# Kernel tuning notes

Hardware: AMD Instinct MI355X
Metric: run time of the kernel (lower is better)

The kernel has to match this reference:

```python
import jax, jax.numpy as jnp
import numpy as np

# Forest of complete L-ary trees, BFS level-contiguous node numbering.
B_TREES, ARITY, DEPTH = 8, 4, 8
C, M, NGEN = 8, 100, 4
COUNTS = [B_TREES * ARITY**l for l in range(DEPTH + 1)]
OFFS = np.concatenate([[0], np.cumsum(COUNTS)]).astype(np.int64)
DIM = int(OFFS[-1])  # 699048
# tree id of each node: within-level index // (ARITY**level)
BATCH = np.concatenate([np.arange(COUNTS[l]) // (ARITY**l) for l in range(DEPTH + 1)])


def setup_inputs() -> dict:
    key = jax.random.key(0)
    k1, k2, k3, k4 = jax.random.split(key, 4)
    return {
        "x": jax.random.randint(k1, (DIM,), 0, M, dtype=jnp.int32),
        "A": jax.random.normal(k2, (C, C, ARITY, NGEN), dtype=jnp.float32) * 2.5,
        "B_emit": jax.random.normal(k3, (C, M, NGEN), dtype=jnp.float32) * 2.5,
        "Pi": jax.random.normal(k4, (C, NGEN), dtype=jnp.float32) * 2.5,
    }


def _htmm_loglik(x, A, B_emit, Pi):
    # softmax reparameterization (matches F.softmax axes in torch code)
    smA = jax.nn.softmax(A, axis=0)            # [C,C,L,G], over child state
    smA_t = jnp.transpose(smA, (2, 0, 1, 3))   # [L,C,C,G]
    smB = jax.nn.softmax(B_emit, axis=1)       # [C,M,G]
    smPi = jax.nn.softmax(Pi, axis=0)          # [C,G]

    # preliminary downward: prior state distribution per node, level by level.
    # Children of a parent are contiguous with sibling position j = idx % ARITY.
    prior_lvls = [jnp.broadcast_to(smPi, (COUNTS[0], C, NGEN))]
    for l in range(1, DEPTH + 1):
        n_pa = COUNTS[l - 1]
        # prior_child[c] = sum_d A[c, d, pos_j, g] * prior_pa[d]
        pl = jnp.einsum('jcdg,pdg->pjcg', smA_t, prior_lvls[-1])
        prior_lvls.append(pl.reshape(n_pa * ARITY, C, NGEN))
    prior = jnp.concatenate(prior_lvls, axis=0)  # [DIM,C,G]

    em = jnp.transpose(smB[:, x], (1, 0, 2))     # [DIM,C,G]
    beta0 = prior * em

    ll = jnp.zeros((DIM, NGEN), dtype=beta0.dtype)
    # leaves = deepest level
    beta_lvl = beta0[OFFS[DEPTH]:OFFS[DEPTH + 1]]
    nu = beta_lvl.sum(1)                          # [n_leaves,G]
    beta_lvl = beta_lvl / nu[:, None, :]
    ll = ll.at[OFFS[DEPTH]:OFFS[DEPTH + 1]].set(jnp.log(nu))

    # upward recursion, bottom-up
    for l in range(DEPTH, 0, -1):
        n_pa = COUNTS[l - 1]
        ratio = (beta_lvl / prior[OFFS[l]:OFFS[l + 1]]).reshape(n_pa, ARITY, C, NGEN)
        # beta_uv[d] = sum_c A[c, d, pos_j, g] * beta_ch[c] / prior_ch[c]
        beta_uv = jnp.einsum('jcdg,pjcg->pjdg', smA_t, ratio)  # [n_pa,L,C,G]
        beta_pa = beta0[OFFS[l - 1]:OFFS[l]] * jnp.prod(beta_uv, axis=1)
        nu = beta_pa.sum(1)
        beta_lvl = beta_pa / nu[:, None, :]
        ll = ll.at[OFFS[l - 1]:OFFS[l]].set(jnp.log(nu))

    # scatter per-node log-likelihood contributions into per-tree totals
    return jax.ops.segment_sum(ll, jnp.asarray(BATCH), num_segments=B_TREES)  # [B_TREES,G]


def reference(x, A, B_emit, Pi):
    return _htmm_loglik(x, A, B_emit, Pi)
```

## Files before the change

### kernel.cpp

```cpp
#include <hip/hip_runtime.h>

constexpr int OFFS1 = 8, OFFS2 = 40, OFFS3 = 168, OFFS4 = 680;
constexpr int OFFS5 = 2728, OFFS6 = 10920, OFFS7 = 43688, OFFS8 = 174760;


#define AG_ST(p, v) __hip_atomic_store((p), (v), __ATOMIC_RELAXED, __HIP_MEMORY_SCOPE_AGENT)
#define AG_LD(p) __hip_atomic_load((p), __ATOMIC_RELAXED, __HIP_MEMORY_SCOPE_AGENT)

template <int CTRL>
static __device__ __forceinline__ float dppmov(float v) {
  return __int_as_float(__builtin_amdgcn_update_dpp(0, __float_as_int(v), CTRL, 0xF, 0xF, true));
}

static __device__ __forceinline__ float bfly8(float v) {
  v += dppmov<0xB1>(v);
  v += dppmov<0x4E>(v);
  v += dppmov<0x141>(v);
  return v;
}

static __device__ __forceinline__ void oct8(float v, float pv[8]) {
  float m = dppmov<0x141>(v);
  pv[0] = dppmov<0x00>(v); pv[1] = dppmov<0x55>(v);
  pv[2] = dppmov<0xAA>(v); pv[3] = dppmov<0xFF>(v);
  pv[4] = dppmov<0x00>(m); pv[5] = dppmov<0x55>(m);
  pv[6] = dppmov<0xAA>(m); pv[7] = dppmov<0xFF>(m);
}

static __device__ __forceinline__ float dot8(const float w[8], const float v[8]) {
  return w[0]*v[0] + w[1]*v[1] + w[2]*v[2] + w[3]*v[3] +
         w[4]*v[4] + w[5]*v[5] + w[6]*v[6] + w[7]*v[7];
}

static __device__ __forceinline__ void ld8(const float* p, float pv[8]) {
  const float4* q = (const float4*)p;
  float4 a = q[0], b = q[1];
  pv[0] = a.x; pv[1] = a.y; pv[2] = a.z; pv[3] = a.w;
  pv[4] = b.x; pv[5] = b.y; pv[6] = b.z; pv[7] = b.w;
}

static __device__ __forceinline__ void ld8p(const float* p, float wp[8], int h) {
  const float4* q = (const float4*)p;
  float4 a = q[h], b = q[1 - h];
  wp[0] = a.x; wp[1] = a.y; wp[2] = a.z; wp[3] = a.w;
  wp[4] = b.w; wp[5] = b.z; wp[6] = b.y; wp[7] = b.x;
}

static __device__ __forceinline__ float dot8p(const float wp[8], const float* p, int h) {
  const float4* q = (const float4*)p;
  float4 a = q[h], b = q[1 - h];
  return wp[0]*a.x + wp[1]*a.y + wp[2]*a.z + wp[3]*a.w +
         wp[4]*b.w + wp[5]*b.z + wp[6]*b.y + wp[7]*b.x;
}

static __device__ __forceinline__ float dot8r(const float w[8], const float* p) {
  const float4* q = (const float4*)p;
  float4 a = q[0], b = q[1];
  return w[0]*a.x + w[1]*a.y + w[2]*a.z + w[3]*a.w +
         w[4]*b.x + w[5]*b.y + w[6]*b.z + w[7]*b.w;
}

static __device__ __forceinline__ float rcpf(float x) { return __builtin_amdgcn_rcpf(x); }

static __device__ __forceinline__ float step_down(const float* wtd_l, float v, int j,
                                                  int r, int h) {
  const float* wb = &wtd_l[j * 256 + r];
  float w[8];
#pragma unroll
  for (int k = 0; k < 4; k++) {
    w[k]     = wb[(4 * h + k) * 32];
    w[4 + k] = wb[(7 - 4 * h - k) * 32];
  }
  float pv[8];
  oct8(v, pv);
  return dot8(w, pv);
}

static __device__ __forceinline__ float upprod(const float wup_p[4][8], const float rat[4]) {
  float prod = 1.f;
#pragma unroll
  for (int j = 0; j < 4; j++) {
    float pr[8];
    oct8(rat[j], pr);
    prod *= dot8(wup_p[j], pr);
  }
  return prod;
}

static __device__ __forceinline__ float leaf7(float u7, float e0, float e1, float e2,
                                              float e3, float em, float* acc) {
  float n0 = bfly8(u7 * e0), n1 = bfly8(u7 * e1);
  float n2 = bfly8(u7 * e2), n3 = bfly8(u7 * e3);
  float p01 = n0 * n1, p23 = n2 * n3;
  float prod = (e0 * e1 * rcpf(p01)) * (e2 * e3 * rcpf(p23));
  *acc += __logf(p01) + __logf(p23);
  float nu7 = bfly8(u7 * em * prod);
  *acc += __logf(nu7);
  return em * prod * rcpf(nu7);
}

__global__ __launch_bounds__(256) void k_all(const int* __restrict__ x,
                                             const float* __restrict__ A,
                                             const float* __restrict__ Bm,
                                             const float* __restrict__ Pi,
                                             float* __restrict__ RAT4,
                                             float* __restrict__ blocksum,
                                             unsigned* __restrict__ ctr,
                                             float* __restrict__ out) {
  __shared__ __align__(16) float wtd_l[1024];
  __shared__ __align__(16) float emt_l[3200];
  __shared__ __align__(16) float pit_l[32];
  __shared__ __align__(16) float etab_l[12800];
  __shared__ __align__(16) float shbuf[2304];
  __shared__ __align__(16) float rat5buf[16][32];
  __shared__ __align__(16) float pri4buf[4][32];
  __shared__ float llb[4];
  __shared__ int lastf;

  int t = threadIdx.x;
  int r = t & 31, g = r >> 3, s = r & 7, grp = t >> 5;
  int h = s >> 2;
  int b = blockIdx.x, tree = b >> 6;

  if (t < 128) {
    int d = t >> 4, j = (t >> 2) & 3, gg = t & 3;
    float v[8], sum = 0.f;
#pragma unroll
    for (int ss = 0; ss < 8; ss++) { v[ss] = __expf(A[((ss * 8 + d) * 4 + j) * 4 + gg]); sum += v[ss]; }
    float inv = rcpf(sum);
#pragma unroll
    for (int ss = 0; ss < 8; ss++) wtd_l[(j * 8 + d) * 32 + gg * 8 + ss] = v[ss] * inv;
  }
  if (t < 4) {
    float v[8], sum = 0.f;
#pragma unroll
    for (int c = 0; c < 8; c++) { v[c] = __expf(Pi[c * 4 + t]); sum += v[c]; }
    float inv = rcpf(sum);
#pragma unroll
    for (int c = 0; c < 8; c++) pit_l[t * 8 + c] = v[c] * inv;
    llb[t] = 0.f;
  }
  {
    int row = t >> 3, part = t & 7, c = row >> 2, gg = row & 3;
    int m0 = part < 4 ? part * 13 : 52 + (part - 4) * 12;
    int mn = part < 4 ? 13 : 12;
    float sum = 0.f;
    for (int m = m0; m < m0 + mn; m++) sum += __expf(Bm[(c * 100 + m) * 4 + gg]);
    sum = bfly8(sum);
    float inv = rcpf(sum);
    for (int m = m0; m < m0 + mn; m++)
      emt_l[m * 32 + gg * 8 + c] = __expf(Bm[(c * 100 + m) * 4 + gg]) * inv;
  }
  __syncthreads();
  {
    int c7 = t & 127, half = t >> 7;
    int j = c7 >> 5, d = (c7 >> 2) & 7, gg = c7 & 3;
    float w[8];
    ld8(&wtd_l[(j * 8 + d) * 32 + gg * 8], w);
    for (int m = half * 50; m < half * 50 + 50; m++)
      etab_l[(m * 4 + j) * 32 + gg * 8 + d] = dot8r(w, &emt_l[m * 32 + gg * 8]);
  }
  float wtd_p[4][8], wup_p[4][8];
#pragma unroll
  for (int j = 0; j < 4; j++) {
    const float* wb = &wtd_l[j * 256 + r];
#pragma unroll
    for (int k = 0; k < 4; k++) {
      wtd_p[j][k]     = wb[(4 * h + k) * 32];
      wtd_p[j][4 + k] = wb[(7 - 4 * h - k) * 32];
    }
    ld8p(&wtd_l[(j * 8 + s) * 32 + g * 8], wup_p[j], h);
  }
  __syncthreads();

  float acc = 0.f;
  {
    int n5A = b * 16 + grp, n5B = n5A + 8;
    const int4* x8A = (const int4*)(x + OFFS8 + n5A * 64);
    const int4* x8B = (const int4*)(x + OFFS8 + n5B * 64);
    const int4* x7A = (const int4*)(x + OFFS7 + n5A * 16);
    const int4* x7B = (const int4*)(x + OFFS7 + n5B * 16);
    int4 x6A = *(const int4*)(x + OFFS6 + n5A * 4);
    int4 x6B = *(const int4*)(x + OFFS6 + n5B * 4);
    int x5A = x[OFFS5 + n5A], x5B = x[OFFS5 + n5B];
    const int* x6aA = (const int*)&x6A;
    const int* x6aB = (const int*)&x6B;

    float vA = pit_l[r], vB = vA, pri4A = 0.f, pri4B = 0.f;
#pragma unroll
    for (int k = 1; k <= 5; k++) {
      vA = step_down(wtd_l, vA, (n5A >> (2 * (5 - k))) & 3, r, h);
      vB = step_down(wtd_l, vB, (n5B >> (2 * (5 - k))) & 3, r, h);
      if (k == 4) { pri4A = vA; pri4B = vB; }
    }
    float pv5A[8], pv5B[8];
    oct8(vA, pv5A); oct8(vB, pv5B);

    float rat6A[4], rat6B[4];
#pragma unroll
    for (int q6 = 0; q6 < 4; q6++) {
      float u6A = dot8(wtd_p[q6], pv5A);
      float u6B = dot8(wtd_p[q6], pv5B);
      float pv6A[8], pv6B[8];
      oct8(u6A, pv6A); oct8(u6B, pv6B);
      int4 x7qA = x7A[q6], x7qB = x7B[q6];
      const int* x7aA = (const int*)&x7qA;
      const int* x7aB = (const int*)&x7qB;

      float rat7A[4], rat7B[4];
#pragma unroll
      for (int q7 = 0; q7 < 4; q7++) {
        int4 xlA = x8A[q6 * 4 + q7], xlB = x8B[q6 * 4 + q7];
        const int* xa = (const int*)&xlA;
        const int* xb = (const int*)&xlB;
        float EA[4], EB[4];
#pragma unroll
        for (int j = 0; j < 4; j++) {
          EA[j] = etab_l[(xa[j] * 4 + j) * 32 + r];
          EB[j] = etab_l[(xb[j] * 4 + j) * 32 + r];
        }
        float u7A = dot8(wtd_p[q7], pv6A);
        float u7B = dot8(wtd_p[q7], pv6B);
        rat7A[q7] = leaf7(u7A, EA[0], EA[1], EA[2], EA[3], emt_l[x7aA[q7] * 32 + r], &acc);
        rat7B[q7] = leaf7(u7B, EB[0], EB[1], EB[2], EB[3], emt_l[x7aB[q7] * 32 + r], &acc);
      }
      float prod6A = upprod(wup_p, rat7A);
      float prod6B = upprod(wup_p, rat7B);
      float em6A = emt_l[x6aA[q6] * 32 + r];
      float em6B = emt_l[x6aB[q6] * 32 + r];
      float nu6A = bfly8(u6A * em6A * prod6A);
      float nu6B = bfly8(u6B * em6B * prod6B);
      acc += __logf(nu6A) + __logf(nu6B);
      rat6A[q6] = em6A * prod6A * rcpf(nu6A);
      rat6B[q6] = em6B * prod6B * rcpf(nu6B);
    }
    float prod5A = upprod(wup_p, rat6A);
    float prod5B = upprod(wup_p, rat6B);
    float em5A = emt_l[x5A * 32 + r], em5B = emt_l[x5B * 32 + r];
    float nu5A = bfly8(vA * em5A * prod5A);
    float nu5B = bfly8(vB * em5B * prod5B);
    acc += __logf(nu5A) + __logf(nu5B);
    rat5buf[grp][r] = em5A * prod5A * rcpf(nu5A);
    rat5buf[8 + grp][r] = em5B * prod5B * rcpf(nu5B);
    if ((grp & 3) == 0) {
      pri4buf[grp >> 2][r] = pri4A;
      pri4buf[2 + (grp >> 2)][r] = pri4B;
    }
  }
  __syncthreads();

  if (grp < 4) {
    int n4 = b * 4 + grp;
    float prod = 1.f;
#pragma unroll
    for (int j = 0; j < 4; j++) prod *= dot8p(wup_p[j], &rat5buf[grp * 4 + j][g * 8], h);
    float em = emt_l[x[OFFS4 + n4] * 32 + r];
    float pr4 = pri4buf[grp][r];
    float nu = bfly8(pr4 * em * prod);
    acc += __logf(nu);
    AG_ST(&RAT4[n4 * 32 + r], em * prod * rcpf(nu));
  }

  if (s == 0) atomicAdd(&llb[g], acc);
  __syncthreads();
  if (t < 4) AG_ST(&blocksum[b * 4 + t], llb[t]);
  asm volatile("s_waitcnt vmcnt(0)" ::: "memory");
  __syncthreads();
  if (t == 0) {
    unsigned old = __hip_atomic_fetch_add(&ctr[tree * 32], 1u, __ATOMIC_RELAXED,
                                          __HIP_MEMORY_SCOPE_AGENT);
    lastf = (old == 63u || old == 0xAAAAAAE9u) ? 1 : 0;
  }
  __syncthreads();
  if (!lastf) return;

  float* rat4_l = etab_l;
#pragma unroll
  for (int ib = 0; ib < 4; ib++) {
    float tmp[8];
#pragma unroll
    for (int i = 0; i < 8; i++) tmp[i] = AG_LD(&RAT4[tree * 8192 + (ib * 8 + i) * 256 + t]);
#pragma unroll
    for (int i = 0; i < 8; i++) rat4_l[(ib * 8 + i) * 256 + t] = tmp[i];
  }
  if (t < 4) llb[t] = 0.f;
  __syncthreads();

  float* st = &shbuf[grp * 288];
  float acc2 = 0.f;
  {
    int n2A = tree * 16 + grp, n2B = n2A + 8;
    int4 x3A = *(const int4*)(x + OFFS3 + n2A * 4);
    int4 x3B = *(const int4*)(x + OFFS3 + n2B * 4);
    int x2A = x[OFFS2 + n2A], x2B = x[OFFS2 + n2B];
    const int* xa = (const int*)&x3A;
    const int* xb = (const int*)&x3B;
    float v2A = pit_l[r], v2B = v2A;
    v2A = step_down(wtd_l, v2A, (n2A >> 2) & 3, r, h);
    v2B = step_down(wtd_l, v2B, (n2B >> 2) & 3, r, h);
    v2A = step_down(wtd_l, v2A, n2A & 3, r, h);
    v2B = step_down(wtd_l, v2B, n2B & 3, r, h);
    float pv2A[8], pv2B[8];
    oct8(v2A, pv2A); oct8(v2B, pv2B);
    float rat3A[4], rat3B[4];
#pragma unroll
    for (int j3 = 0; j3 < 4; j3++) {
      int i3A = grp * 4 + j3, i3B = (8 + grp) * 4 + j3;
      float p3A = dot8(wtd_p[j3], pv2A);
      float p3B = dot8(wtd_p[j3], pv2B);
      float prodA = 1.f, prodB = 1.f;
#pragma unroll
      for (int j = 0; j < 4; j++) {
        prodA *= dot8p(wup_p[j], &rat4_l[(i3A * 4 + j) * 32 + g * 8], h);
        prodB *= dot8p(wup_p[j], &rat4_l[(i3B * 4 + j) * 32 + g * 8], h);
      }
      float emA = emt_l[xa[j3] * 32 + r], emB = emt_l[xb[j3] * 32 + r];
      float nuA = bfly8(p3A * emA * prodA), nuB = bfly8(p3B * emB * prodB);
      acc2 += __logf(nuA) + __logf(nuB);
      rat3A[j3] = emA * prodA * rcpf(nuA);
      rat3B[j3] = emB * prodB * rcpf(nuB);
    }
    float prodA = upprod(wup_p, rat3A);
    float prodB = upprod(wup_p, rat3B);
    float emA = emt_l[x2A * 32 + r], emB = emt_l[x2B * 32 + r];
    float nuA = bfly8(v2A * emA * prodA), nuB = bfly8(v2B * emB * prodB);
    acc2 += __logf(nuA) + __logf(nuB);
    st[5 * 32 + r] = emA * prodA * rcpf(nuA);
    st[6 * 32 + r] = emB * prodB * rcpf(nuB);
  }
  __syncthreads();
  if (grp < 4) {
    int n1g = tree * 4 + grp;
    float pv[8];
    ld8(pit_l + g * 8, pv);
    float v1 = 0.f;
#pragma unroll
    for (int d = 0; d < 8; d++) v1 += wtd_l[(grp * 8 + d) * 32 + r] * pv[d];
    float prod = 1.f;
#pragma unroll
    for (int j = 0; j < 4; j++) {
      int l2 = grp * 4 + j;
      prod *= dot8p(wup_p[j], &shbuf[(l2 & 7) * 288 + (5 + (l2 >> 3)) * 32 + g * 8], h);
    }
    float em = emt_l[x[OFFS1 + n1g] * 32 + r];
    float nu = bfly8(v1 * em * prod);
    acc2 += __logf(nu);
    st[7 * 32 + r] = em * prod * rcpf(nu);
  }
  __syncthreads();
  if (grp == 0) {
    float pr = pit_l[r];
    float prod = 1.f;
#pragma unroll
    for (int j = 0; j < 4; j++) prod *= dot8p(wup_p[j], &shbuf[j * 288 + 7 * 32 + g * 8], h);
    float em = emt_l[x[tree] * 32 + r];
    float nu = bfly8(pr * em * prod);
    acc2 += __logf(nu);
  }
  __syncthreads();
  if (s == 0) atomicAdd(&llb[g], acc2);
  float v = AG_LD(&blocksum[tree * 256 + t]);
  __syncthreads();
  shbuf[t] = v;
  __syncthreads();
#pragma unroll
  for (int off = 128; off >= 4; off >>= 1) {
    if (t < off) shbuf[t] += shbuf[t + off];
    __syncthreads();
  }
  if (t < 4) out[tree * 4 + t] = shbuf[t] + llb[t];
}

extern "C" void kernel_launch(void* const* d_in, const int* in_sizes, int n_in,
                              void* d_out, int out_size, void* d_ws, size_t ws_size,
                              hipStream_t stream) {
  const int* x = (const int*)d_in[0];
  const float* A = (const float*)d_in[1];
  const float* Bm = (const float*)d_in[2];
  const float* Pi = (const float*)d_in[3];
  float* ws = (float*)d_ws;
  unsigned* ctr = (unsigned*)d_ws;
  float* blocksum = ws + 256;
  float* RAT4 = ws + 256 + 2048;
  float* out = (float*)d_out;

  k_all<<<512, 256, 0, stream>>>(x, A, Bm, Pi, RAT4, blocksum, ctr, out);
}
```

Baseline: 103.5 us.

## Drop precomputed leaf emission table; compute leaf terms on the fly

Removes the per-block precomputed etab table (transition times emission over all symbols) and its build phase plus a block-wide barrier. Leaf emission terms are now computed inline as an 8-wide dot of the upward weights with the emission row. This cuts shared memory use (allowing more occupancy) and the setup work, at the cost of extra FMAs and LDS reads per leaf. The final-block RAT4 load is also restructured into a smaller staging buffer processed in two halves.

After: 91.49 us. 11.6% less time.

```diff
diff --git a/kernel.cpp b/kernel.cpp
--- a/kernel.cpp
+++ b/kernel.cpp
@@ -51,13 +51,6 @@
   float4 a = q[h], b = q[1 - h];
   return wp[0]*a.x + wp[1]*a.y + wp[2]*a.z + wp[3]*a.w +
          wp[4]*b.w + wp[5]*b.z + wp[6]*b.y + wp[7]*b.x;
-}
-
-static __device__ __forceinline__ float dot8r(const float w[8], const float* p) {
-  const float4* q = (const float4*)p;
-  float4 a = q[0], b = q[1];
-  return w[0]*a.x + w[1]*a.y + w[2]*a.z + w[3]*a.w +
-         w[4]*b.x + w[5]*b.y + w[6]*b.z + w[7]*b.w;
 }
 
 static __device__ __forceinline__ float rcpf(float x) { return __builtin_amdgcn_rcpf(x); }
@@ -110,7 +103,7 @@
   __shared__ __align__(16) float wtd_l[1024];
   __shared__ __align__(16) float emt_l[3200];
   __shared__ __align__(16) float pit_l[32];
-  __shared__ __align__(16) float etab_l[12800];
+  __shared__ __align__(16) float stg[4096];
   __shared__ __align__(16) float shbuf[2304];
   __shared__ __align__(16) float rat5buf[16][32];
   __shared__ __align__(16) float pri4buf[4][32];
@@ -120,6 +113,7 @@
   int t = threadIdx.x;
   int r = t & 31, g = r >> 3, s = r & 7, grp = t >> 5;
   int h = s >> 2;
+  int gb = g * 8;
   int b = blockIdx.x, tree = b >> 6;
 
   if (t < 128) {
@@ -152,14 +146,6 @@
       emt_l[m * 32 + gg * 8 + c] = __expf(Bm[(c * 100 + m) * 4 + gg]) * inv;
   }
   __syncthreads();
-  {
-    int c7 = t & 127, half = t >> 7;
-    int j = c7 >> 5, d = (c7 >> 2) & 7, gg = c7 & 3;
-    float w[8];
-    ld8(&wtd_l[(j * 8 + d) * 32 + gg * 8], w);
-    for (int m = half * 50; m < half * 50 + 50; m++)
-      etab_l[(m * 4 + j) * 32 + gg * 8 + d] = dot8r(w, &emt_l[m * 32 + gg * 8]);
-  }
   float wtd_p[4][8], wup_p[4][8];
 #pragma unroll
   for (int j = 0; j < 4; j++) {
@@ -169,9 +155,8 @@
       wtd_p[j][k]     = wb[(4 * h + k) * 32];
       wtd_p[j][4 + k] = wb[(7 - 4 * h - k) * 32];
     }
-    ld8p(&wtd_l[(j * 8 + s) * 32 + g * 8], wup_p[j], h);
-  }
-  __syncthreads();
+    ld8p(&wtd_l[(j * 8 + s) * 32 + gb], wup_p[j], h);
+  }
 
   float acc = 0.f;
   {
@@ -216,8 +201,8 @@
         float EA[4], EB[4];
 #pragma unroll
         for (int j = 0; j < 4; j++) {
-          EA[j] = etab_l[(xa[j] * 4 + j) * 32 + r];
-          EB[j] = etab_l[(xb[j] * 4 + j) * 32 + r];
+          EA[j] = dot8p(wup_p[j], &emt_l[xa[j] * 32 + gb], h);
+          EB[j] = dot8p(wup_p[j], &emt_l[xb[j] * 32 + gb], h);
         }
         float u7A = dot8(wtd_p[q7], pv6A);
         float u7B = dot8(wtd_p[q7], pv6B);
@@ -253,7 +238,7 @@
     int n4 = b * 4 + grp;
     float prod = 1.f;
 #pragma unroll
-    for (int j = 0; j < 4; j++) prod *= dot8p(wup_p[j], &rat5buf[grp * 4 + j][g * 8], h);
+    for (int j = 0; j < 4; j++) prod *= dot8p(wup_p[j], &rat5buf[grp * 4 + j][gb], h);
     float em = emt_l[x[OFFS4 + n4] * 32 + r];
     float pr4 = pri4buf[grp][r];
     float nu = bfly8(pr4 * em * prod);
@@ -274,65 +259,85 @@
   __syncthreads();
   if (!lastf) return;
 
-  float* rat4_l = etab_l;
-#pragma unroll
-  for (int ib = 0; ib < 4; ib++) {
-    float tmp[8];
-#pragma unroll
-    for (int i = 0; i < 8; i++) tmp[i] = AG_LD(&RAT4[tree * 8192 + (ib * 8 + i) * 256 + t]);
-#pragma unroll
-    for (int i = 0; i < 8; i++) rat4_l[(ib * 8 + i) * 256 + t] = tmp[i];
-  }
+  float tmpA[16], tmpB[16];
+#pragma unroll
+  for (int i = 0; i < 16; i++) tmpA[i] = AG_LD(&RAT4[tree * 8192 + i * 256 + t]);
+#pragma unroll
+  for (int i = 0; i < 16; i++) stg[i * 256 + t] = tmpA[i];
+#pragma unroll
+  for (int i = 0; i < 16; i++) tmpB[i] = AG_LD(&RAT4[tree * 8192 + 4096 + i * 256 + t]);
   if (t < 4) llb[t] = 0.f;
   __syncthreads();
 
   float* st = &shbuf[grp * 288];
   float acc2 = 0.f;
   {
-    int n2A = tree * 16 + grp, n2B = n2A + 8;
+    int n2A = tree * 16 + grp;
     int4 x3A = *(const int4*)(x + OFFS3 + n2A * 4);
+    int x2A = x[OFFS2 + n2A];
+    const int* xa = (const int*)&x3A;
+    float v2A = pit_l[r];
+    v2A = step_down(wtd_l, v2A, (n2A >> 2) & 3, r, h);
+    v2A = step_down(wtd_l, v2A, n2A & 3, r, h);
+    float pv2A[8];
+    oct8(v2A, pv2A);
+    float rat3A[4];
+#pragma unroll
+    for (int j3 = 0; j3 < 4; j3++) {
+      float p3A = dot8(wtd_p[j3], pv2A);
+      float prodA = 1.f;
+#pragma unroll
+      for (int j = 0; j < 4; j++)
+        prodA *= dot8p(wup_p[j], &stg[(grp * 16 + j3 * 4 + j) * 32 + gb], h);
+      float emA = emt_l[xa[j3] * 32 + r];
+      float nuA = bfly8(p3A * emA * prodA);
+      acc2 += __logf(nuA);
+      rat3A[j3] = emA * prodA * rcpf(nuA);
+    }
+    float prodA = upprod(wup_p, rat3A);
+    float emA = emt_l[x2A * 32 + r];
+    float nuA = bfly8(v2A * emA * prodA);
+    acc2 += __logf(nuA);
+    st[5 * 32 + r] = emA * prodA * rcpf(nuA);
+  }
+  __syncthreads();
+#pragma unroll
+  for (int i = 0; i < 16; i++) stg[i * 256 + t] = tmpB[i];
+  __syncthreads();
+  {
+    int n2B = tree * 16 + 8 + grp;
     int4 x3B = *(const int4*)(x + OFFS3 + n2B * 4);
-    int x2A = x[OFFS2 + n2A], x2B = x[OFFS2 + n2B];
-    const int* xa = (const int*)&x3A;
+    int x2B = x[OFFS2 + n2B];
     const int* xb = (const int*)&x3B;
-    float v2A = pit_l[r], v2B = v2A;
-    v2A = step_down(wtd_l, v2A, (n2A >> 2) & 3, r, h);
+    float v2B = pit_l[r];
     v2B = step_down(wtd_l, v2B, (n2B >> 2) & 3, r, h);
-    v2A = step_down(wtd_l, v2A, n2A & 3, r, h);
     v2B = step_down(wtd_l, v2B, n2B & 3, r, h);
-    float pv2A[8], pv2B[8];
-    oct8(v2A, pv2A); oct8(v2B, pv2B);
-    float rat3A[4], rat3B[4];
+    float pv2B[8];
+    oct8(v2B, pv2B);
+    float rat3B[4];
 #pragma unroll
     for (int j3 = 0; j3 < 4; j3++) {
-      int i3A = grp * 4 + j3, i3B = (8 + grp) * 4 + j3;
-      float p3A = dot8(wtd_p[j3], pv2A);
       float p3B = dot8(wtd_p[j3], pv2B);
-      float prodA = 1.f, prodB = 1.f;
-#pragma unroll
-      for (int j = 0; j < 4; j++) {
-        prodA *= dot8p(wup_p[j], &rat4_l[(i3A * 4 + j) * 32 + g * 8], h);
-        prodB *= dot8p(wup_p[j], &rat4_l[(i3B * 4 + j) * 32 + g * 8], h);
-      }
-      float emA = emt_l[xa[j3] * 32 + r], emB = emt_l[xb[j3] * 32 + r];
-      float nuA = bfly8(p3A * emA * prodA), nuB = bfly8(p3B * emB * prodB);
-      acc2 += __logf(nuA) + __logf(nuB);
-      rat3A[j3] = emA * prodA * rcpf(nuA);
+      float prodB = 1.f;
+#pragma unroll
+      for (int j = 0; j < 4; j++)
+        prodB *= dot8p(wup_p[j], &stg[(grp * 16 + j3 * 4 + j) * 32 + gb], h);
+      float emB = emt_l[xb[j3] * 32 + r];
+      float nuB = bfly8(p3B * emB * prodB);
+      acc2 += __logf(nuB);
       rat3B[j3] = emB * prodB * rcpf(nuB);
     }
-    float prodA = upprod(wup_p, rat3A);
     float prodB = upprod(wup_p, rat3B);
-    float emA = emt_l[x2A * 32 + r], emB = emt_l[x2B * 32 + r];
-    float nuA = bfly8(v2A * emA * prodA), nuB = bfly8(v2B * emB * prodB);
-    acc2 += __logf(nuA) + __logf(nuB);
-    st[5 * 32 + r] = emA * prodA * rcpf(nuA);
+    float emB = emt_l[x2B * 32 + r];
+    float nuB = bfly8(v2B * emB * prodB);
+    acc2 += __logf(nuB);
     st[6 * 32 + r] = emB * prodB * rcpf(nuB);
   }
   __syncthreads();
   if (grp < 4) {
     int n1g = tree * 4 + grp;
     float pv[8];
-    ld8(pit_l + g * 8, pv);
+    ld8(pit_l + gb, pv);
     float v1 = 0.f;
 #pragma unroll
     for (int d = 0; d < 8; d++) v1 += wtd_l[(grp * 8 + d) * 32 + r] * pv[d];
@@ -340,7 +345,7 @@
 #pragma unroll
     for (int j = 0; j < 4; j++) {
       int l2 = grp * 4 + j;
-      prod *= dot8p(wup_p[j], &shbuf[(l2 & 7) * 288 + (5 + (l2 >> 3)) * 32 + g * 8], h);
+      prod *= dot8p(wup_p[j], &shbuf[(l2 & 7) * 288 + (5 + (l2 >> 3)) * 32 + gb], h);
     }
     float em = emt_l[x[OFFS1 + n1g] * 32 + r];
     float nu = bfly8(v1 * em * prod);
@@ -352,7 +357,7 @@
     float pr = pit_l[r];
     float prod = 1.f;
 #pragma unroll
-    for (int j = 0; j < 4; j++) prod *= dot8p(wup_p[j], &shbuf[j * 288 + 7 * 32 + g * 8], h);
+    for (int j = 0; j < 4; j++) prod *= dot8p(wup_p[j], &shbuf[j * 288 + 7 * 32 + gb], h);
     float em = emt_l[x[tree] * 32 + r];
     float nu = bfly8(pr * em * prod);
     acc2 += __logf(nu);
```

## Split fused kernel into two launches and drop per-block emission-transition table

Applied to the files above, without the earlier changes.

Replaces the single kernel, which used an atomic counter so the last block per tree ran the top levels, with two kernel launches: a 512-block phase for the lower levels and an 8-block phase for the top of each tree. The per-block 12800-entry etab table is removed and leaf emission-transition terms are computed on the fly with dot8p over the emission table. This cuts LDS use and table-build time per block and may improve occupancy. In exchange it adds leaf-level arithmetic and a second launch, and phase 2 rebuilds the softmax tables.

Result: faster. 94.66 us (-8.6%).

```diff
diff --git a/kernel.cpp b/kernel.cpp
--- a/kernel.cpp
+++ b/kernel.cpp
@@ -3,9 +3,6 @@
 constexpr int OFFS1 = 8, OFFS2 = 40, OFFS3 = 168, OFFS4 = 680;
 constexpr int OFFS5 = 2728, OFFS6 = 10920, OFFS7 = 43688, OFFS8 = 174760;
 
-
-#define AG_ST(p, v) __hip_atomic_store((p), (v), __ATOMIC_RELAXED, __HIP_MEMORY_SCOPE_AGENT)
-#define AG_LD(p) __hip_atomic_load((p), __ATOMIC_RELAXED, __HIP_MEMORY_SCOPE_AGENT)
 
 template <int CTRL>
 static __device__ __forceinline__ float dppmov(float v) {
@@ -51,13 +48,6 @@
   float4 a = q[h], b = q[1 - h];
   return wp[0]*a.x + wp[1]*a.y + wp[2]*a.z + wp[3]*a.w +
          wp[4]*b.w + wp[5]*b.z + wp[6]*b.y + wp[7]*b.x;
-}
-
-static __device__ __forceinline__ float dot8r(const float w[8], const float* p) {
-  const float4* q = (const float4*)p;
-  float4 a = q[0], b = q[1];
-  return w[0]*a.x + w[1]*a.y + w[2]*a.z + w[3]*a.w +
-         w[4]*b.x + w[5]*b.y + w[6]*b.z + w[7]*b.w;
 }
 
 static __device__ __forceinline__ float rcpf(float x) { return __builtin_amdgcn_rcpf(x); }
@@ -99,29 +89,11 @@
   return em * prod * rcpf(nu7);
 }
 
-__global__ __launch_bounds__(256) void k_all(const int* __restrict__ x,
-                                             const float* __restrict__ A,
-                                             const float* __restrict__ Bm,
-                                             const float* __restrict__ Pi,
-                                             float* __restrict__ RAT4,
-                                             float* __restrict__ blocksum,
-                                             unsigned* __restrict__ ctr,
-                                             float* __restrict__ out) {
-  __shared__ __align__(16) float wtd_l[1024];
-  __shared__ __align__(16) float emt_l[3200];
-  __shared__ __align__(16) float pit_l[32];
-  __shared__ __align__(16) float etab_l[12800];
-  __shared__ __align__(16) float shbuf[2304];
-  __shared__ __align__(16) float rat5buf[16][32];
-  __shared__ __align__(16) float pri4buf[4][32];
-  __shared__ float llb[4];
-  __shared__ int lastf;
-
-  int t = threadIdx.x;
-  int r = t & 31, g = r >> 3, s = r & 7, grp = t >> 5;
-  int h = s >> 2;
-  int b = blockIdx.x, tree = b >> 6;
-
+static __device__ __forceinline__ void build_tables(const float* __restrict__ A,
+                                                    const float* __restrict__ Bm,
+                                                    const float* __restrict__ Pi,
+                                                    float* wtd_l, float* emt_l,
+                                                    float* pit_l, float* llb, int t) {
   if (t < 128) {
     int d = t >> 4, j = (t >> 2) & 3, gg = t & 3;
     float v[8], sum = 0.f;
@@ -151,15 +123,28 @@
     for (int m = m0; m < m0 + mn; m++)
       emt_l[m * 32 + gg * 8 + c] = __expf(Bm[(c * 100 + m) * 4 + gg]) * inv;
   }
-  __syncthreads();
-  {
-    int c7 = t & 127, half = t >> 7;
-    int j = c7 >> 5, d = (c7 >> 2) & 7, gg = c7 & 3;
-    float w[8];
-    ld8(&wtd_l[(j * 8 + d) * 32 + gg * 8], w);
-    for (int m = half * 50; m < half * 50 + 50; m++)
-      etab_l[(m * 4 + j) * 32 + gg * 8 + d] = dot8r(w, &emt_l[m * 32 + gg * 8]);
-  }
+}
+
+__global__ __launch_bounds__(256) void k_phase1(const int* __restrict__ x,
+                                                const float* __restrict__ A,
+                                                const float* __restrict__ Bm,
+                                                const float* __restrict__ Pi,
+                                                float* __restrict__ RAT4,
+                                                float* __restrict__ blocksum) {
+  __shared__ __align__(16) float wtd_l[1024];
+  __shared__ __align__(16) float emt_l[3200];
+  __shared__ __align__(16) float pit_l[32];
+  __shared__ __align__(16) float rat5buf[16][32];
+  __shared__ __align__(16) float pri4buf[4][32];
+  __shared__ float llb[4];
+
+  int t = threadIdx.x;
+  int r = t & 31, g = r >> 3, s = r & 7, grp = t >> 5;
+  int h = s >> 2, gb = g * 8;
+  int b = blockIdx.x;
+
+  build_tables(A, Bm, Pi, wtd_l, emt_l, pit_l, llb, t);
+  __syncthreads();
   float wtd_p[4][8], wup_p[4][8];
 #pragma unroll
   for (int j = 0; j < 4; j++) {
@@ -169,9 +154,8 @@
       wtd_p[j][k]     = wb[(4 * h + k) * 32];
       wtd_p[j][4 + k] = wb[(7 - 4 * h - k) * 32];
     }
-    ld8p(&wtd_l[(j * 8 + s) * 32 + g * 8], wup_p[j], h);
-  }
-  __syncthreads();
+    ld8p(&wtd_l[(j * 8 + s) * 32 + gb], wup_p[j], h);
+  }
 
   float acc = 0.f;
   {
@@ -216,8 +200,8 @@
         float EA[4], EB[4];
 #pragma unroll
         for (int j = 0; j < 4; j++) {
-          EA[j] = etab_l[(xa[j] * 4 + j) * 32 + r];
-          EB[j] = etab_l[(xb[j] * 4 + j) * 32 + r];
+          EA[j] = dot8p(wup_p[j], &emt_l[xa[j] * 32 + gb], h);
+          EB[j] = dot8p(wup_p[j], &emt_l[xb[j] * 32 + gb], h);
         }
         float u7A = dot8(wtd_p[q7], pv6A);
         float u7B = dot8(wtd_p[q7], pv6B);
@@ -253,40 +237,59 @@
     int n4 = b * 4 + grp;
     float prod = 1.f;
 #pragma unroll
-    for (int j = 0; j < 4; j++) prod *= dot8p(wup_p[j], &rat5buf[grp * 4 + j][g * 8], h);
+    for (int j = 0; j < 4; j++) prod *= dot8p(wup_p[j], &rat5buf[grp * 4 + j][gb], h);
     float em = emt_l[x[OFFS4 + n4] * 32 + r];
     float pr4 = pri4buf[grp][r];
     float nu = bfly8(pr4 * em * prod);
     acc += __logf(nu);
-    AG_ST(&RAT4[n4 * 32 + r], em * prod * rcpf(nu));
+    RAT4[n4 * 32 + r] = em * prod * rcpf(nu);
   }
 
   if (s == 0) atomicAdd(&llb[g], acc);
   __syncthreads();
-  if (t < 4) AG_ST(&blocksum[b * 4 + t], llb[t]);
-  asm volatile("s_waitcnt vmcnt(0)" ::: "memory");
-  __syncthreads();
-  if (t == 0) {
-    unsigned old = __hip_atomic_fetch_add(&ctr[tree * 32], 1u, __ATOMIC_RELAXED,
-                                          __HIP_MEMORY_SCOPE_AGENT);
-    lastf = (old == 63u || old == 0xAAAAAAE9u) ? 1 : 0;
-  }
-  __syncthreads();
-  if (!lastf) return;
-
-  float* rat4_l = etab_l;
-#pragma unroll
-  for (int ib = 0; ib < 4; ib++) {
-    float tmp[8];
-#pragma unroll
-    for (int i = 0; i < 8; i++) tmp[i] = AG_LD(&RAT4[tree * 8192 + (ib * 8 + i) * 256 + t]);
-#pragma unroll
-    for (int i = 0; i < 8; i++) rat4_l[(ib * 8 + i) * 256 + t] = tmp[i];
-  }
-  if (t < 4) llb[t] = 0.f;
-  __syncthreads();
-
-  float* st = &shbuf[grp * 288];
+  if (t < 4) blocksum[b * 4 + t] = llb[t];
+}
+
+__global__ __launch_bounds__(256) void k_phase2(const int* __restrict__ x,
+                                                const float* __restrict__ A,
+                                                const float* __restrict__ Bm,
+                                                const float* __restrict__ Pi,
+                                                const float* __restrict__ RAT4,
+                                                const float* __restrict__ blocksum,
+                                                float* __restrict__ out) {
+  __shared__ __align__(16) float wtd_l[1024];
+  __shared__ __align__(16) float emt_l[3200];
+  __shared__ __align__(16) float pit_l[32];
+  __shared__ __align__(16) float stg[8192];
+  __shared__ __align__(16) float xb[640];
+  __shared__ float llb[4];
+
+  int t = threadIdx.x;
+  int r = t & 31, g = r >> 3, s = r & 7, grp = t >> 5;
+  int h = s >> 2, gb = g * 8;
+  int tree = blockIdx.x;
+
+  build_tables(A, Bm, Pi, wtd_l, emt_l, pit_l, llb, t);
+  {
+    const float4* src = (const float4*)(RAT4 + tree * 8192);
+    float4* dst = (float4*)stg;
+#pragma unroll
+    for (int i = 0; i < 8; i++) dst[i * 256 + t] = src[i * 256 + t];
+  }
+  __syncthreads();
+
+  float wtd_p[4][8], wup_p[4][8];
+#pragma unroll
+  for (int j = 0; j < 4; j++) {
+    const float* wb = &wtd_l[j * 256 + r];
+#pragma unroll
+    for (int k = 0; k < 4; k++) {
+      wtd_p[j][k]     = wb[(4 * h + k) * 32];
+      wtd_p[j][4 + k] = wb[(7 - 4 * h - k) * 32];
+    }
+    ld8p(&wtd_l[(j * 8 + s) * 32 + gb], wup_p[j], h);
+  }
+
   float acc2 = 0.f;
   {
     int n2A = tree * 16 + grp, n2B = n2A + 8;
@@ -294,7 +297,7 @@
     int4 x3B = *(const int4*)(x + OFFS3 + n2B * 4);
     int x2A = x[OFFS2 + n2A], x2B = x[OFFS2 + n2B];
     const int* xa = (const int*)&x3A;
-    const int* xb = (const int*)&x3B;
+    const int* xbv = (const int*)&x3B;
     float v2A = pit_l[r], v2B = v2A;
     v2A = step_down(wtd_l, v2A, (n2A >> 2) & 3, r, h);
     v2B = step_down(wtd_l, v2B, (n2B >> 2) & 3, r, h);
@@ -311,10 +314,10 @@
       float prodA = 1.f, prodB = 1.f;
 #pragma unroll
       for (int j = 0; j < 4; j++) {
-        prodA *= dot8p(wup_p[j], &rat4_l[(i3A * 4 + j) * 32 + g * 8], h);
-        prodB *= dot8p(wup_p[j], &rat4_l[(i3B * 4 + j) * 32 + g * 8], h);
+        prodA *= dot8p(wup_p[j], &stg[(i3A * 4 + j) * 32 + gb], h);
+        prodB *= dot8p(wup_p[j], &stg[(i3B * 4 + j) * 32 + gb], h);
       }
-      float emA = emt_l[xa[j3] * 32 + r], emB = emt_l[xb[j3] * 32 + r];
+      float emA = emt_l[xa[j3] * 32 + r], emB = emt_l[xbv[j3] * 32 + r];
       float nuA = bfly8(p3A * emA * prodA), nuB = bfly8(p3B * emB * prodB);
       acc2 += __logf(nuA) + __logf(nuB);
       rat3A[j3] = emA * prodA * rcpf(nuA);
@@ -325,50 +328,43 @@
     float emA = emt_l[x2A * 32 + r], emB = emt_l[x2B * 32 + r];
     float nuA = bfly8(v2A * emA * prodA), nuB = bfly8(v2B * emB * prodB);
     acc2 += __logf(nuA) + __logf(nuB);
-    st[5 * 32 + r] = emA * prodA * rcpf(nuA);
-    st[6 * 32 + r] = emB * prodB * rcpf(nuB);
+    xb[grp * 32 + r] = emA * prodA * rcpf(nuA);
+    xb[(8 + grp) * 32 + r] = emB * prodB * rcpf(nuB);
   }
   __syncthreads();
   if (grp < 4) {
     int n1g = tree * 4 + grp;
-    float pv[8];
-    ld8(pit_l + g * 8, pv);
-    float v1 = 0.f;
-#pragma unroll
-    for (int d = 0; d < 8; d++) v1 += wtd_l[(grp * 8 + d) * 32 + r] * pv[d];
+    float v1 = step_down(wtd_l, pit_l[r], grp, r, h);
     float prod = 1.f;
 #pragma unroll
-    for (int j = 0; j < 4; j++) {
-      int l2 = grp * 4 + j;
-      prod *= dot8p(wup_p[j], &shbuf[(l2 & 7) * 288 + (5 + (l2 >> 3)) * 32 + g * 8], h);
-    }
+    for (int j = 0; j < 4; j++) prod *= dot8p(wup_p[j], &xb[(grp * 4 + j) * 32 + gb], h);
     float em = emt_l[x[OFFS1 + n1g] * 32 + r];
     float nu = bfly8(v1 * em * prod);
     acc2 += __logf(nu);
-    st[7 * 32 + r] = em * prod * rcpf(nu);
+    xb[512 + grp * 32 + r] = em * prod * rcpf(nu);
   }
   __syncthreads();
   if (grp == 0) {
     float pr = pit_l[r];
     float prod = 1.f;
 #pragma unroll
-    for (int j = 0; j < 4; j++) prod *= dot8p(wup_p[j], &shbuf[j * 288 + 7 * 32 + g * 8], h);
+    for (int j = 0; j < 4; j++) prod *= dot8p(wup_p[j], &xb[512 + j * 32 + gb], h);
     float em = emt_l[x[tree] * 32 + r];
     float nu = bfly8(pr * em * prod);
     acc2 += __logf(nu);
   }
   __syncthreads();
   if (s == 0) atomicAdd(&llb[g], acc2);
-  float v = AG_LD(&blocksum[tree * 256 + t]);
-  __syncthreads();
-  shbuf[t] = v;
+  float v = blocksum[tree * 256 + t];
+  __syncthreads();
+  stg[t] = v;
   __syncthreads();
 #pragma unroll
   for (int off = 128; off >= 4; off >>= 1) {
-    if (t < off) shbuf[t] += shbuf[t + off];
+    if (t < off) stg[t] += stg[t + off];
     __syncthreads();
   }
-  if (t < 4) out[tree * 4 + t] = shbuf[t] + llb[t];
+  if (t < 4) out[tree * 4 + t] = stg[t] + llb[t];
 }
 
 extern "C" void kernel_launch(void* const* d_in, const int* in_sizes, int n_in,
@@ -379,10 +375,10 @@
   const float* Bm = (const float*)d_in[2];
   const float* Pi = (const float*)d_in[3];
   float* ws = (float*)d_ws;
-  unsigned* ctr = (unsigned*)d_ws;
   float* blocksum = ws + 256;
   float* RAT4 = ws + 256 + 2048;
   float* out = (float*)d_out;
 
-  k_all<<<512, 256, 0, stream>>>(x, A, Bm, Pi, RAT4, blocksum, ctr, out);
-}
+  k_phase1<<<512, 256, 0, stream>>>(x, A, Bm, Pi, RAT4, blocksum);
+  k_phase2<<<8, 256, 0, stream>>>(x, A, Bm, Pi, RAT4, blocksum, out);
+}
```
